# Performance work log

Hardware: AMD Instinct MI355X
Metric: run time of the kernel (lower is better)

## Reference

```python
import jax, jax.numpy as jnp
import numpy as np
import math

N_HEADS = 32
N_REP = 4
N_KV = N_HEADS // N_REP
HEAD_DIM = 128
MAX_SEQ = 4096
BATCH = 8
Q_LEN = 1


def setup_inputs() -> dict:
    key = jax.random.key(0)
    ks = jax.random.split(key, 7)
    input_pos = jax.random.randint(ks[0], (Q_LEN,), 0, MAX_SEQ, dtype=jnp.int32)
    q = jax.random.normal(ks[1], (N_HEADS, BATCH, Q_LEN, HEAD_DIM), dtype=jnp.float32)
    k = jax.random.normal(ks[2], (N_KV, BATCH, Q_LEN, HEAD_DIM), dtype=jnp.float32)
    v = jax.random.normal(ks[3], (N_KV, BATCH, Q_LEN, HEAD_DIM), dtype=jnp.float32)
    k_cache = jax.random.normal(ks[4], (N_KV, BATCH, MAX_SEQ, HEAD_DIM), dtype=jnp.float32)
    v_cache = jax.random.normal(ks[5], (N_KV, BATCH, MAX_SEQ, HEAD_DIM), dtype=jnp.float32)
    mask = jax.random.normal(ks[6], (MAX_SEQ, MAX_SEQ), dtype=jnp.float32)
    return {"input_pos": input_pos, "q": q, "k": k, "v": v,
            "k_cache": k_cache, "v_cache": v_cache, "mask": mask}


def reference(input_pos, q, k, v, k_cache, v_cache, mask):
    # KV cache update (index_put_ at positions input_pos along seq axis)
    kc = k_cache.at[:, :, input_pos, :].set(k)   # [G, B, S, D]
    vc = v_cache.at[:, :, input_pos, :].set(v)   # [G, B, S, D]
    scale = 1.0 / math.sqrt(HEAD_DIM)
    # group query heads by kv head: head i uses kv group i // n_rep
    qg = q.reshape(N_KV, N_REP, BATCH, Q_LEN, HEAD_DIM)
    scores = jnp.einsum('grbqd,gbsd->grbqs', qg, kc) * scale
    scores = scores + mask[input_pos]            # [Q, S] broadcast
    probs = jax.nn.softmax(scores, axis=-1)
    out = jnp.einsum('grbqs,gbsd->grbqd', probs, vc)  # [G, R, B, Q, D]
    # torch.cat over heads (i = g*n_rep + r) on last dim -> [B, Q, H*D]
    out = out.transpose(2, 3, 0, 1, 4).reshape(BATCH, Q_LEN, N_HEADS * HEAD_DIM)
    return out
```

## Files before the change

kernel.cpp:

```cpp
#include <hip/hip_runtime.h>
#include <math.h>

#define NKV    8
#define NREP   4
#define NH     32
#define BATCH  8
#define D      128
#define SEQ    4096
#define CHUNKS 32
#define CS     128
#define HROWS  64
#define PSTRIDE 130

__device__ __forceinline__ void stage16(const float* src, float* lds_dst) {
    __builtin_amdgcn_global_load_lds(
        (const __attribute__((address_space(1))) void*)src,
        (__attribute__((address_space(3))) void*)lds_dst,
        16, 0, 0);
}

__global__ __launch_bounds__(256, 4) void attn_partial(
    const int*   __restrict__ input_pos,
    const float* __restrict__ q,
    const float* __restrict__ knew,
    const float* __restrict__ vnew,
    const float* __restrict__ kcache,
    const float* __restrict__ vcache,
    const float* __restrict__ mask,
    float*       __restrict__ ws)
{
    const int pair = blockIdx.x;
    const int c    = blockIdx.y;
    const int g    = pair >> 3;
    const int b    = pair & 7;
    const int t    = threadIdx.x;
    const int w    = t >> 6;
    const int lane = t & 63;
    const int p4   = lane >> 4;
    const int l16  = lane & 15;
    const int vh   = lane >> 5;
    const int l32  = lane & 31;
    const int pos  = input_pos[0];

    __shared__ __align__(16) float buf[HROWS * D];
    __shared__ float sc[NREP][CS];
    __shared__ float ml[NREP][2];
    float (*opart)[NREP][D] = (float (*)[NREP][D])buf;

    const float  scale  = 0.08838834764831845f;
    const size_t kvbase = (size_t)(g * BATCH + b) * SEQ * D;
    const float* kbase  = kcache + kvbase;
    const float* vbase  = vcache + kvbase;
    const float* mrow   = mask + (size_t)pos * SEQ;
    const float* knewr  = knew + (size_t)(g * BATCH + b) * D;
    const float* vnewr  = vnew + (size_t)(g * BATCH + b) * D;
    const int    s0     = c * CS;

    float4 qv[NREP][2];
    #pragma unroll
    for (int r = 0; r < NREP; ++r) {
        const float4* qr = (const float4*)(q + ((size_t)(g * NREP + r) * BATCH + b) * D
                                           + l16 * 8);
        qv[r][0] = qr[0];
        qv[r][1] = qr[1];
    }

    auto stage_half = [&](const float* base, const float* newrow, int hh) {
        #pragma unroll
        for (int jj = 0; jj < 8; ++jj) {
            const int j  = w * 8 + jj;
            const int rl = 2 * j + vh;
            const int s  = s0 + hh * HROWS + rl;
            const float* src = ((s == pos) ? newrow : (base + (size_t)s * D)) + l32 * 4;
            stage16(src, &buf[j * 256]);
        }
    };

    auto scores_half = [&](int hh) {
        #pragma unroll
        for (int i = 0; i < 4; ++i) {
            const int rl = w * 16 + i * 4 + p4;
            const int sl = hh * HROWS + rl;
            const float4* kr = (const float4*)&buf[rl * D + l16 * 8];
            const float4 k0 = kr[0], k1 = kr[1];
            float acc[NREP];
            #pragma unroll
            for (int r = 0; r < NREP; ++r) {
                float a;
                a = k0.x * qv[r][0].x;
                a = fmaf(k0.y, qv[r][0].y, a);
                a = fmaf(k0.z, qv[r][0].z, a);
                a = fmaf(k0.w, qv[r][0].w, a);
                a = fmaf(k1.x, qv[r][1].x, a);
                a = fmaf(k1.y, qv[r][1].y, a);
                a = fmaf(k1.z, qv[r][1].z, a);
                a = fmaf(k1.w, qv[r][1].w, a);
                acc[r] = a;
            }
            #pragma unroll
            for (int off = 1; off < 16; off <<= 1) {
                #pragma unroll
                for (int r = 0; r < NREP; ++r)
                    acc[r] += __shfl_xor(acc[r], off);
            }
            if (l16 == 0) {
                const float mval = mrow[s0 + sl];
                #pragma unroll
                for (int r = 0; r < NREP; ++r)
                    sc[r][sl] = acc[r] * scale + mval;
            }
        }
    };

    stage_half(kbase, knewr, 0);
    __syncthreads();
    scores_half(0);
    __syncthreads();
    stage_half(kbase, knewr, 1);
    __syncthreads();
    scores_half(1);
    __syncthreads();

    stage_half(vbase, vnewr, 0);

    {
        const int r = w;
        float v0 = sc[r][lane];
        float v1 = sc[r][lane + 64];
        float m  = fmaxf(v0, v1);
        #pragma unroll
        for (int off = 1; off < 64; off <<= 1)
            m = fmaxf(m, __shfl_xor(m, off));
        float e0 = __expf(v0 - m);
        float e1 = __expf(v1 - m);
        sc[r][lane]      = e0;
        sc[r][lane + 64] = e1;
        float l = e0 + e1;
        #pragma unroll
        for (int off = 1; off < 64; off <<= 1)
            l += __shfl_xor(l, off);
        if (lane == 0) { ml[r][0] = m; ml[r][1] = l; }
    }
    __syncthreads();

    float4 oacc[NREP];
    #pragma unroll
    for (int r = 0; r < NREP; ++r) oacc[r] = make_float4(0.f, 0.f, 0.f, 0.f);

    auto pv_half = [&](int hh) {
        #pragma unroll
        for (int it = 0; it < 8; ++it) {
            const int rl = w * 16 + it * 2 + vh;
            const int sl = hh * HROWS + rl;
            const float4 v4 = *(const float4*)&buf[rl * D + l32 * 4];
            #pragma unroll
            for (int r = 0; r < NREP; ++r) {
                const float pr = sc[r][sl];
                oacc[r].x = fmaf(pr, v4.x, oacc[r].x);
                oacc[r].y = fmaf(pr, v4.y, oacc[r].y);
                oacc[r].z = fmaf(pr, v4.z, oacc[r].z);
                oacc[r].w = fmaf(pr, v4.w, oacc[r].w);
            }
        }
    };

    pv_half(0);
    __syncthreads();
    stage_half(vbase, vnewr, 1);
    __syncthreads();
    pv_half(1);

    #pragma unroll
    for (int r = 0; r < NREP; ++r) {
        oacc[r].x += __shfl_xor(oacc[r].x, 32);
        oacc[r].y += __shfl_xor(oacc[r].y, 32);
        oacc[r].z += __shfl_xor(oacc[r].z, 32);
        oacc[r].w += __shfl_xor(oacc[r].w, 32);
    }
    __syncthreads();
    if (vh == 0) {
        #pragma unroll
        for (int r = 0; r < NREP; ++r)
            *(float4*)&opart[w][r][l32 * 4] = oacc[r];
    }
    __syncthreads();

    #pragma unroll
    for (int ii = 0; ii < 2; ++ii) {
        int idx = t + ii * 256;
        int r   = idx >> 7;
        int d   = idx & 127;
        float sum = opart[0][r][d] + opart[1][r][d]
                  + opart[2][r][d] + opart[3][r][d];
        size_t base = (((size_t)pair * CHUNKS + c) * NREP + r) * PSTRIDE;
        ws[base + d] = sum;
        if (d == 0) { ws[base + 128] = ml[r][0]; ws[base + 129] = ml[r][1]; }
    }
}

__global__ __launch_bounds__(128) void attn_reduce(
    const float* __restrict__ ws, float* __restrict__ out)
{
    const int idx  = blockIdx.x;
    const int pair = idx >> 2;
    const int r    = idx & 3;
    const int g    = pair >> 3;
    const int b    = pair & 7;
    const int d    = threadIdx.x;

    float mv[CHUNKS], lv[CHUNKS];
    float M = -INFINITY;
    #pragma unroll
    for (int c = 0; c < CHUNKS; ++c) {
        size_t base = (((size_t)pair * CHUNKS + c) * NREP + r) * PSTRIDE;
        float2 t = *(const float2*)&ws[base + 128];
        mv[c] = t.x; lv[c] = t.y;
        M = fmaxf(M, t.x);
    }
    float acc = 0.f, L = 0.f;
    #pragma unroll
    for (int c = 0; c < CHUNKS; ++c) {
        size_t base = (((size_t)pair * CHUNKS + c) * NREP + r) * PSTRIDE;
        float wgt = __expf(mv[c] - M);
        acc += ws[base + d] * wgt;
        L   += lv[c] * wgt;
    }
    int h = g * NREP + r;
    out[(size_t)b * (NH * D) + h * D + d] = acc / L;
}

__global__ __launch_bounds__(256) void attn_full(
    const int*   __restrict__ input_pos,
    const float* __restrict__ q,
    const float* __restrict__ knew,
    const float* __restrict__ vnew,
    const float* __restrict__ kcache,
    const float* __restrict__ vcache,
    const float* __restrict__ mask,
    float*       __restrict__ out)
{
    const int idx = blockIdx.x;
    const int h   = idx >> 3;
    const int b   = idx & 7;
    const int g   = h >> 2;
    const int t   = threadIdx.x;
    const int wave = t >> 6, lane = t & 63, half = lane >> 5, l32 = lane & 31;
    const int pos = input_pos[0];

    __shared__ float sc[SEQ];
    __shared__ float wred[4];
    __shared__ float oacc[2][D];

    const size_t kvbase = (size_t)(g * BATCH + b) * SEQ * D;
    const float* kbase  = kcache + kvbase;
    const float* vbase  = vcache + kvbase;
    const float* mrow   = mask + (size_t)pos * SEQ;
    const float* knewr  = knew + (size_t)(g * BATCH + b) * D;
    const float* vnewr  = vnew + (size_t)(g * BATCH + b) * D;
    const float  scale  = 0.08838834764831845f;

    float4 qv = ((const float4*)(q + (size_t)(h * BATCH + b) * D))[l32];

    for (int p = 0; p < SEQ / 8; ++p) {
        int s = p * 8 + wave * 2 + half;
        const float4* krow = (s == pos) ? (const float4*)knewr
                                        : (const float4*)(kbase + (size_t)s * D);
        float4 kv = krow[l32];
        float acc = qv.x * kv.x + qv.y * kv.y + qv.z * kv.z + qv.w * kv.w;
        #pragma unroll
        for (int off = 1; off < 32; off <<= 1)
            acc += __shfl_xor(acc, off);
        if (l32 == 0) sc[s] = acc * scale + mrow[s];
    }
    __syncthreads();

    float m = -INFINITY;
    for (int s = t; s < SEQ; s += 256) m = fmaxf(m, sc[s]);
    #pragma unroll
    for (int off = 1; off < 64; off <<= 1) m = fmaxf(m, __shfl_xor(m, off));
    if (lane == 0) wred[wave] = m;
    __syncthreads();
    m = fmaxf(fmaxf(wred[0], wred[1]), fmaxf(wred[2], wred[3]));
    __syncthreads();

    float l = 0.f;
    for (int s = t; s < SEQ; s += 256) { float e = __expf(sc[s] - m); sc[s] = e; l += e; }
    #pragma unroll
    for (int off = 1; off < 64; off <<= 1) l += __shfl_xor(l, off);
    __syncthreads();
    if (lane == 0) wred[wave] = l;
    __syncthreads();
    float L = wred[0] + wred[1] + wred[2] + wred[3];

    {
        int hf = t >> 7, d = t & 127;
        float acc = 0.f;
        for (int s = hf * (SEQ / 2); s < (hf + 1) * (SEQ / 2); ++s) {
            const float* vrow = (s == pos) ? vnewr : (vbase + (size_t)s * D);
            acc += sc[s] * vrow[d];
        }
        oacc[hf][d] = acc;
    }
    __syncthreads();
    if (t < D) out[(size_t)b * (NH * D) + h * D + t] = (oacc[0][t] + oacc[1][t]) / L;
}

extern "C" void kernel_launch(void* const* d_in, const int* in_sizes, int n_in,
                              void* d_out, int out_size, void* d_ws, size_t ws_size,
                              hipStream_t stream) {
    const int*   input_pos = (const int*)  d_in[0];
    const float* q         = (const float*)d_in[1];
    const float* k         = (const float*)d_in[2];
    const float* v         = (const float*)d_in[3];
    const float* kcache    = (const float*)d_in[4];
    const float* vcache    = (const float*)d_in[5];
    const float* mask      = (const float*)d_in[6];
    float* out = (float*)d_out;

    const size_t need = (size_t)64 * CHUNKS * NREP * PSTRIDE * sizeof(float);
    if (ws_size >= need) {
        dim3 g1(64, CHUNKS);
        attn_partial<<<g1, 256, 0, stream>>>(input_pos, q, k, v, kcache, vcache, mask,
                                             (float*)d_ws);
        attn_reduce<<<256, 128, 0, stream>>>((const float*)d_ws, out);
    } else {
        attn_full<<<256, 256, 0, stream>>>(input_pos, q, k, v, kcache, vcache, mask, out);
    }
}
```

Measured before the change: 52.75 us.

## Pipeline K/V staging with triple-buffered LDS and larger sequence chunks

Replaces the serial stage-then-compute halves with a 16-stage loop over 32-row tiles that streams K then V through a three-slot LDS ring. Each tile's global-to-LDS copy is issued two stages ahead and guarded by explicit vmcnt waits and barriers. Chunk size doubles to 256 rows, which halves the grid and the partial results the reduce kernel must combine. The mask row is preloaded into the score buffer up front. Occupancy hint drops to 3 blocks per CU, and the hand-written waitcnt counts must match the number of loads issued per stage.

```diff
diff --git a/kernel.cpp b/kernel.cpp
--- a/kernel.cpp
+++ b/kernel.cpp
@@ -7,9 +7,10 @@
 #define BATCH  8
 #define D      128
 #define SEQ    4096
-#define CHUNKS 32
-#define CS     128
-#define HROWS  64
+#define CHUNKS 16
+#define CS     256
+#define SR     32
+#define NSTAGE 16
 #define PSTRIDE 130
 
 __device__ __forceinline__ void stage16(const float* src, float* lds_dst) {
@@ -19,7 +20,7 @@
         16, 0, 0);
 }
 
-__global__ __launch_bounds__(256, 4) void attn_partial(
+__global__ __launch_bounds__(256, 3) void attn_partial(
     const int*   __restrict__ input_pos,
     const float* __restrict__ q,
     const float* __restrict__ knew,
@@ -42,16 +43,15 @@
     const int l32  = lane & 31;
     const int pos  = input_pos[0];
 
-    __shared__ __align__(16) float buf[HROWS * D];
+    __shared__ __align__(16) float buf[3][SR * D];
     __shared__ float sc[NREP][CS];
     __shared__ float ml[NREP][2];
-    float (*opart)[NREP][D] = (float (*)[NREP][D])buf;
+    float (*opart)[NREP][D] = (float (*)[NREP][D])&buf[1][0];
 
     const float  scale  = 0.08838834764831845f;
     const size_t kvbase = (size_t)(g * BATCH + b) * SEQ * D;
     const float* kbase  = kcache + kvbase;
     const float* vbase  = vcache + kvbase;
-    const float* mrow   = mask + (size_t)pos * SEQ;
     const float* knewr  = knew + (size_t)(g * BATCH + b) * D;
     const float* vnewr  = vnew + (size_t)(g * BATCH + b) * D;
     const int    s0     = c * CS;
@@ -64,111 +64,126 @@
         qv[r][0] = qr[0];
         qv[r][1] = qr[1];
     }
-
-    auto stage_half = [&](const float* base, const float* newrow, int hh) {
+    {
+        const float mreg = mask[(size_t)pos * SEQ + s0 + t];
         #pragma unroll
-        for (int jj = 0; jj < 8; ++jj) {
-            const int j  = w * 8 + jj;
-            const int rl = 2 * j + vh;
-            const int s  = s0 + hh * HROWS + rl;
-            const float* src = ((s == pos) ? newrow : (base + (size_t)s * D)) + l32 * 4;
-            stage16(src, &buf[j * 256]);
+        for (int r = 0; r < NREP; ++r) sc[r][t] = mreg;
+    }
+
+    auto stage_one = [&](int st, int bi_) {
+        const float* base = (st < 8) ? kbase : vbase;
+        const float* nrow = (st < 8) ? knewr : vnewr;
+        const int    r0   = s0 + (st & 7) * SR;
+        #pragma unroll
+        for (int jj = 0; jj < 4; ++jj) {
+            const int j = (w << 2) + jj;
+            const int s = r0 + 2 * j + vh;
+            const float* src = ((s == pos) ? nrow : (base + (size_t)s * D)) + l32 * 4;
+            stage16(src, &buf[bi_][j * 256]);
         }
     };
 
-    auto scores_half = [&](int hh) {
-        #pragma unroll
-        for (int i = 0; i < 4; ++i) {
-            const int rl = w * 16 + i * 4 + p4;
-            const int sl = hh * HROWS + rl;
-            const float4* kr = (const float4*)&buf[rl * D + l16 * 8];
-            const float4 k0 = kr[0], k1 = kr[1];
-            float acc[NREP];
+    float4 oacc[NREP];
+    #pragma unroll
+    for (int r = 0; r < NREP; ++r) oacc[r] = make_float4(0.f, 0.f, 0.f, 0.f);
+
+    stage_one(0, 0);
+    stage_one(1, 1);
+
+    int bi = 0;
+    #pragma unroll
+    for (int st = 0; st < NSTAGE; ++st) {
+        if (st < NSTAGE - 1) {
+            asm volatile("s_waitcnt vmcnt(4) lgkmcnt(0)" ::: "memory");
+        } else {
+            asm volatile("s_waitcnt vmcnt(0) lgkmcnt(0)" ::: "memory");
+        }
+        __builtin_amdgcn_s_barrier();
+
+        if (st == 8) {
+            const int r = w;
+            float v0 = sc[r][lane];
+            float v1 = sc[r][lane + 64];
+            float v2 = sc[r][lane + 128];
+            float v3 = sc[r][lane + 192];
+            float m = fmaxf(fmaxf(v0, v1), fmaxf(v2, v3));
             #pragma unroll
-            for (int r = 0; r < NREP; ++r) {
-                float a;
-                a = k0.x * qv[r][0].x;
-                a = fmaf(k0.y, qv[r][0].y, a);
-                a = fmaf(k0.z, qv[r][0].z, a);
-                a = fmaf(k0.w, qv[r][0].w, a);
-                a = fmaf(k1.x, qv[r][1].x, a);
-                a = fmaf(k1.y, qv[r][1].y, a);
-                a = fmaf(k1.z, qv[r][1].z, a);
-                a = fmaf(k1.w, qv[r][1].w, a);
-                acc[r] = a;
+            for (int off = 1; off < 64; off <<= 1)
+                m = fmaxf(m, __shfl_xor(m, off));
+            float e0 = __expf(v0 - m);
+            float e1 = __expf(v1 - m);
+            float e2 = __expf(v2 - m);
+            float e3 = __expf(v3 - m);
+            sc[r][lane]       = e0;
+            sc[r][lane + 64]  = e1;
+            sc[r][lane + 128] = e2;
+            sc[r][lane + 192] = e3;
+            float L = (e0 + e1) + (e2 + e3);
+            #pragma unroll
+            for (int off = 1; off < 64; off <<= 1)
+                L += __shfl_xor(L, off);
+            if (lane == 0) { ml[r][0] = m; ml[r][1] = L; }
+            asm volatile("s_waitcnt lgkmcnt(0)" ::: "memory");
+            __builtin_amdgcn_s_barrier();
+        }
+
+        if (st + 2 < NSTAGE) {
+            int b2 = bi + 2; if (b2 >= 3) b2 -= 3;
+            stage_one(st + 2, b2);
+        }
+
+        if (st < 8) {
+            #pragma unroll
+            for (int i = 0; i < 2; ++i) {
+                const int rl = (w << 3) + (i << 2) + p4;
+                const int sl = (st << 5) + rl;
+                const float4* kr = (const float4*)&buf[bi][rl * D + l16 * 8];
+                const float4 k0 = kr[0], k1 = kr[1];
+                float acc[NREP];
+                #pragma unroll
+                for (int r = 0; r < NREP; ++r) {
+                    float a;
+                    a = k0.x * qv[r][0].x;
+                    a = fmaf(k0.y, qv[r][0].y, a);
+                    a = fmaf(k0.z, qv[r][0].z, a);
+                    a = fmaf(k0.w, qv[r][0].w, a);
+                    a = fmaf(k1.x, qv[r][1].x, a);
+                    a = fmaf(k1.y, qv[r][1].y, a);
+                    a = fmaf(k1.z, qv[r][1].z, a);
+                    a = fmaf(k1.w, qv[r][1].w, a);
+                    acc[r] = a;
+                }
+                #pragma unroll
+                for (int off = 1; off < 16; off <<= 1) {
+                    #pragma unroll
+                    for (int r = 0; r < NREP; ++r)
+                        acc[r] += __shfl_xor(acc[r], off);
+                }
+                if (l16 == 0) {
+                    #pragma unroll
+                    for (int r = 0; r < NREP; ++r)
+                        sc[r][sl] = fmaf(acc[r], scale, sc[r][sl]);
+                }
             }
+        } else {
+            const int vt = st - 8;
             #pragma unroll
-            for (int off = 1; off < 16; off <<= 1) {
+            for (int it = 0; it < 4; ++it) {
+                const int rl = (w << 3) + (it << 1) + vh;
+                const int sl = (vt << 5) + rl;
+                const float4 v4 = *(const float4*)&buf[bi][rl * D + l32 * 4];
                 #pragma unroll
-                for (int r = 0; r < NREP; ++r)
-                    acc[r] += __shfl_xor(acc[r], off);
+                for (int r = 0; r < NREP; ++r) {
+                    const float pr = sc[r][sl];
+                    oacc[r].x = fmaf(pr, v4.x, oacc[r].x);
+                    oacc[r].y = fmaf(pr, v4.y, oacc[r].y);
+                    oacc[r].z = fmaf(pr, v4.z, oacc[r].z);
+                    oacc[r].w = fmaf(pr, v4.w, oacc[r].w);
+                }
             }
-            if (l16 == 0) {
-                const float mval = mrow[s0 + sl];
-                #pragma unroll
-                for (int r = 0; r < NREP; ++r)
-                    sc[r][sl] = acc[r] * scale + mval;
-            }
-        }
-    };
-
-    stage_half(kbase, knewr, 0);
-    __syncthreads();
-    scores_half(0);
-    __syncthreads();
-    stage_half(kbase, knewr, 1);
-    __syncthreads();
-    scores_half(1);
-    __syncthreads();
-
-    stage_half(vbase, vnewr, 0);
-
-    {
-        const int r = w;
-        float v0 = sc[r][lane];
-        float v1 = sc[r][lane + 64];
-        float m  = fmaxf(v0, v1);
-        #pragma unroll
-        for (int off = 1; off < 64; off <<= 1)
-            m = fmaxf(m, __shfl_xor(m, off));
-        float e0 = __expf(v0 - m);
-        float e1 = __expf(v1 - m);
-        sc[r][lane]      = e0;
-        sc[r][lane + 64] = e1;
-        float l = e0 + e1;
-        #pragma unroll
-        for (int off = 1; off < 64; off <<= 1)
-            l += __shfl_xor(l, off);
-        if (lane == 0) { ml[r][0] = m; ml[r][1] = l; }
-    }
-    __syncthreads();
-
-    float4 oacc[NREP];
-    #pragma unroll
-    for (int r = 0; r < NREP; ++r) oacc[r] = make_float4(0.f, 0.f, 0.f, 0.f);
-
-    auto pv_half = [&](int hh) {
-        #pragma unroll
-        for (int it = 0; it < 8; ++it) {
-            const int rl = w * 16 + it * 2 + vh;
-            const int sl = hh * HROWS + rl;
-            const float4 v4 = *(const float4*)&buf[rl * D + l32 * 4];
-            #pragma unroll
-            for (int r = 0; r < NREP; ++r) {
-                const float pr = sc[r][sl];
-                oacc[r].x = fmaf(pr, v4.x, oacc[r].x);
-                oacc[r].y = fmaf(pr, v4.y, oacc[r].y);
-                oacc[r].z = fmaf(pr, v4.z, oacc[r].z);
-                oacc[r].w = fmaf(pr, v4.w, oacc[r].w);
-            }
-        }
-    };
-
-    pv_half(0);
-    __syncthreads();
-    stage_half(vbase, vnewr, 1);
-    __syncthreads();
-    pv_half(1);
+        }
+        if (++bi == 3) bi = 0;
+    }
 
     #pragma unroll
     for (int r = 0; r < NREP; ++r) {
@@ -177,13 +192,13 @@
         oacc[r].z += __shfl_xor(oacc[r].z, 32);
         oacc[r].w += __shfl_xor(oacc[r].w, 32);
     }
-    __syncthreads();
     if (vh == 0) {
         #pragma unroll
         for (int r = 0; r < NREP; ++r)
             *(float4*)&opart[w][r][l32 * 4] = oacc[r];
     }
-    __syncthreads();
+    asm volatile("s_waitcnt lgkmcnt(0)" ::: "memory");
+    __builtin_amdgcn_s_barrier();
 
     #pragma unroll
     for (int ii = 0; ii < 2; ++ii) {
```

Measured after the change: 58.32 us. 10.6% more time.
